# Performance work log

Hardware: AMD Instinct MI355X
Metric: run time of the kernel (lower is better)

## Reference

```python
import jax, jax.numpy as jnp
import numpy as np
import math

B, N, D_IN, D_OUT, H = 8, 1024, 512, 512, 8
DH = D_OUT // H  # 64
SCALE = math.sqrt(DH)

def setup_inputs() -> dict:
    key = jax.random.key(0)
    ks = jax.random.split(key, 10)
    s_in = 1.0 / math.sqrt(D_IN)
    s_out = 1.0 / math.sqrt(D_OUT)
    return {
        "x": jax.random.normal(ks[0], (B, N, D_IN), dtype=jnp.float32),
        "Wq": jax.random.uniform(ks[1], (D_IN, D_OUT), jnp.float32, -s_in, s_in),
        "bq": jnp.zeros((D_OUT,), jnp.float32),
        "Wk": jax.random.uniform(ks[2], (D_IN, D_OUT), jnp.float32, -s_in, s_in),
        "bk": jnp.zeros((D_OUT,), jnp.float32),
        "Wv": jax.random.uniform(ks[3], (D_IN, D_OUT), jnp.float32, -s_in, s_in),
        "bv": jnp.zeros((D_OUT,), jnp.float32),
        "Wo": jax.random.uniform(ks[4], (D_OUT, D_OUT), jnp.float32, -s_out, s_out),
        "bo": jnp.zeros((D_OUT,), jnp.float32),
        # external distance-based positional bias buffer (num_heads, N, N)
        "pos_bias": 0.01 * jax.random.normal(ks[5], (H, N, N), dtype=jnp.float32),
    }

def reference(x, Wq, bq, Wk, bk, Wv, bv, Wo, bo, pos_bias):
    Bx, Nx, _ = x.shape
    # QKV projections -> (B, H, N, DH)
    def split_heads(t):
        return t.reshape(Bx, Nx, H, DH).transpose(0, 2, 1, 3)
    q = split_heads(x @ Wq + bq)
    k = split_heads(x @ Wk + bk)
    v = split_heads(x @ Wv + bv)
    # scaled dot-product scores with additive positional bias
    scores = jnp.einsum('bhnd,bhmd->bhnm', q, k) / SCALE + pos_bias[None]
    attn = jax.nn.softmax(scores, axis=-1)  # dropout p=0 (eval)
    out = jnp.einsum('bhnm,bhmd->bhnd', attn, v)
    out = out.transpose(0, 2, 1, 3).reshape(Bx, Nx, D_OUT)  # concat heads
    return out @ Wo + bo
```

## Files before the change

### kernel.cpp

```cpp
#include <hip/hip_runtime.h>
#include <hip/hip_bf16.h>
#include <stdint.h>


typedef __attribute__((ext_vector_type(4))) float f32x4;
typedef __attribute__((ext_vector_type(8))) short s16x8;
typedef __attribute__((ext_vector_type(4))) unsigned short u16x4;
typedef __attribute__((ext_vector_type(8))) unsigned short u16x8;

union FragAB { s16x8 v; u16x4 h[2]; unsigned u[4]; };

#define LOG2E 1.44269504089f
#define QSCALE (0.125f * LOG2E)

__device__ __forceinline__ unsigned short f2b(float f) {
  unsigned u = __builtin_bit_cast(unsigned, f);
  u = (u + 0x7FFFu + ((u >> 16) & 1u)) >> 16;
  return (unsigned short)u;
}
__device__ __forceinline__ unsigned pack2(float lo, float hi) {
  return ((unsigned)f2b(hi) << 16) | (unsigned)f2b(lo);
}

__global__ __launch_bounds__(256) void prep_k(const float* __restrict__ x,
                                              unsigned short* __restrict__ xb,
                                              const float* __restrict__ W0,
                                              const float* __restrict__ W1,
                                              const float* __restrict__ W2,
                                              const float* __restrict__ W3,
                                              unsigned short* __restrict__ Wt) {
  __shared__ float ld[64][68];
  const int t = threadIdx.x;
  if (blockIdx.x < 4096) {
    int idx = blockIdx.x * 256 + t;
    f32x4 v = ((const f32x4*)x)[idx];
    u16x4 o;
#pragma unroll
    for (int j = 0; j < 4; j++) o[j] = f2b(v[j]);
    ((u16x4*)xb)[idx] = o;
    return;
  }
  const int bid2 = blockIdx.x - 4096;
  const int widx = bid2 >> 6;
  const int tile = bid2 & 63;
  const int trow = tile >> 3, tcol = tile & 7;
  const float* W = widx == 0 ? W0 : widx == 1 ? W1 : widx == 2 ? W2 : W3;
  const int r = t >> 2, cc = (t & 3) * 16;
  const float* src = W + (size_t)(trow * 64 + r) * 512 + tcol * 64 + cc;
#pragma unroll
  for (int u = 0; u < 4; u++)
    ((f32x4*)&ld[r][cc])[u] = ((const f32x4*)src)[u];
  __syncthreads();
  unsigned short* dst = Wt + ((size_t)widx << 18) + (size_t)(tcol * 64 + r) * 512 +
                        trow * 64 + cc;
#pragma unroll
  for (int u = 0; u < 4; u++) {
    u16x4 o;
#pragma unroll
    for (int e = 0; e < 4; e++) o[e] = f2b(ld[cc + u * 4 + e][r]);
    ((u16x4*)dst)[u] = o;
  }
}

__global__ __launch_bounds__(256, 2) void gemm_qkv_k(const unsigned short* __restrict__ A,
                                                     const unsigned short* __restrict__ Bt,
                                                     const float* __restrict__ bq,
                                                     const float* __restrict__ bk,
                                                     const float* __restrict__ bv,
                                                     unsigned short* __restrict__ outp) {
  __shared__ unsigned short At[2][128][36];
  __shared__ unsigned short Bts[2][128][36];
  const int tid = threadIdx.x;
  const int lane = tid & 63;
  const int w = tid >> 6;
  const int wm = w >> 1, wn = w & 1;
  const int g = lane >> 4, c = lane & 15;
  const int bn0 = (blockIdx.x % 12) * 128;
  const int bm0 = (blockIdx.x / 12) * 128;
  const int srow = tid >> 1;
  const int scol = (tid & 1) * 16;

  f32x4 acc[4][4];
#pragma unroll
  for (int i = 0; i < 4; i++)
#pragma unroll
    for (int j = 0; j < 4; j++) acc[i][j] = f32x4{0.f, 0.f, 0.f, 0.f};

  u16x4 ra[4], rb[4];
  auto ld = [&](int kt) {
    const u16x4* pa = (const u16x4*)(A + (size_t)(bm0 + srow) * 512 + kt * 32 + scol);
    const u16x4* pb = (const u16x4*)(Bt + (size_t)(bn0 + srow) * 512 + kt * 32 + scol);
#pragma unroll
    for (int j = 0; j < 4; j++) { ra[j] = pa[j]; rb[j] = pb[j]; }
  };
  auto st = [&](int b) {
    u16x4* da = (u16x4*)&At[b][srow][scol];
    u16x4* db = (u16x4*)&Bts[b][srow][scol];
#pragma unroll
    for (int j = 0; j < 4; j++) { da[j] = ra[j]; db[j] = rb[j]; }
  };

  ld(0); st(0);
  __syncthreads();

  for (int kt = 0; kt < 16; ++kt) {
    const int cb = kt & 1;
    if (kt < 15) ld(kt + 1);

    FragAB af[4], bf[4];
#pragma unroll
    for (int mi = 0; mi < 4; mi++) {
      const u16x4* p = (const u16x4*)&At[cb][wm * 64 + mi * 16 + c][g * 8];
      af[mi].h[0] = p[0]; af[mi].h[1] = p[1];
    }
#pragma unroll
    for (int ni = 0; ni < 4; ni++) {
      const u16x4* p = (const u16x4*)&Bts[cb][wn * 64 + ni * 16 + c][g * 8];
      bf[ni].h[0] = p[0]; bf[ni].h[1] = p[1];
    }
    __builtin_amdgcn_s_setprio(1);
#pragma unroll
    for (int mi = 0; mi < 4; mi++)
#pragma unroll
      for (int ni = 0; ni < 4; ni++)
        acc[mi][ni] = __builtin_amdgcn_mfma_f32_16x16x32_bf16(af[mi].v, bf[ni].v,
                                                              acc[mi][ni], 0, 0, 0);
    __builtin_amdgcn_s_setprio(0);

    if (kt < 15) {
      st(cb ^ 1);
      __syncthreads();
    }
  }

  const int qkv = (bn0 + wn * 64) >> 9;
  const float* bp = qkv == 0 ? bq : (qkv == 1 ? bk : bv);
  const float scale = qkv == 0 ? QSCALE : 1.0f;
#pragma unroll
  for (int mi = 0; mi < 4; mi++) {
#pragma unroll
    for (int ni = 0; ni < 4; ni++) {
      const int col = bn0 + wn * 64 + ni * 16 + c;
      const int c9 = col & 511;
      const float bvv = bp[c9];
#pragma unroll
      for (int m = 0; m < 4; m++) {
        const int row = bm0 + wm * 64 + mi * 16 + g * 4 + m;
        const float v = (acc[mi][ni][m] + bvv) * scale;
        const int b = row >> 10, n = row & 1023;
        const int hh = c9 >> 6, d = col & 63;
        outp[((size_t)qkv << 22) + ((size_t)((b << 3) + hh) << 16) +
             ((size_t)n << 6) + d] = f2b(v);
      }
    }
  }
}

__global__ __launch_bounds__(256, 2) void gemm_o_k(const unsigned short* __restrict__ A,
                                                   const unsigned short* __restrict__ Bt,
                                                   const float* __restrict__ bias,
                                                   float* __restrict__ outp) {
  __shared__ unsigned short At[2][128][36];
  __shared__ unsigned short Bts[2][128][36];
  const int tid = threadIdx.x;
  const int lane = tid & 63;
  const int w = tid >> 6;
  const int wm = w >> 1, wn = w & 1;
  const int g = lane >> 4, c = lane & 15;
  const int bn0 = (blockIdx.x & 3) * 128;
  const int bm0 = (blockIdx.x >> 2) * 128;
  const int srow = tid >> 1;
  const int scol = (tid & 1) * 16;

  f32x4 acc[4][4];
#pragma unroll
  for (int i = 0; i < 4; i++)
#pragma unroll
    for (int j = 0; j < 4; j++) acc[i][j] = f32x4{0.f, 0.f, 0.f, 0.f};

  u16x4 ra[4], rb[4];
  auto ld = [&](int kt) {
    const u16x4* pa = (const u16x4*)(A + (size_t)(bm0 + srow) * 512 + kt * 32 + scol);
    const u16x4* pb = (const u16x4*)(Bt + (size_t)(bn0 + srow) * 512 + kt * 32 + scol);
#pragma unroll
    for (int j = 0; j < 4; j++) { ra[j] = pa[j]; rb[j] = pb[j]; }
  };
  auto st = [&](int b) {
    u16x4* da = (u16x4*)&At[b][srow][scol];
    u16x4* db = (u16x4*)&Bts[b][srow][scol];
#pragma unroll
    for (int j = 0; j < 4; j++) { da[j] = ra[j]; db[j] = rb[j]; }
  };

  ld(0); st(0);
  __syncthreads();

  for (int kt = 0; kt < 16; ++kt) {
    const int cb = kt & 1;
    if (kt < 15) ld(kt + 1);

    FragAB af[4], bf[4];
#pragma unroll
    for (int mi = 0; mi < 4; mi++) {
      const u16x4* p = (const u16x4*)&At[cb][wm * 64 + mi * 16 + c][g * 8];
      af[mi].h[0] = p[0]; af[mi].h[1] = p[1];
    }
#pragma unroll
    for (int ni = 0; ni < 4; ni++) {
      const u16x4* p = (const u16x4*)&Bts[cb][wn * 64 + ni * 16 + c][g * 8];
      bf[ni].h[0] = p[0]; bf[ni].h[1] = p[1];
    }
    __builtin_amdgcn_s_setprio(1);
#pragma unroll
    for (int mi = 0; mi < 4; mi++)
#pragma unroll
      for (int ni = 0; ni < 4; ni++)
        acc[mi][ni] = __builtin_amdgcn_mfma_f32_16x16x32_bf16(af[mi].v, bf[ni].v,
                                                              acc[mi][ni], 0, 0, 0);
    __builtin_amdgcn_s_setprio(0);

    if (kt < 15) {
      st(cb ^ 1);
      __syncthreads();
    }
  }

#pragma unroll
  for (int mi = 0; mi < 4; mi++) {
#pragma unroll
    for (int ni = 0; ni < 4; ni++) {
      const int col = bn0 + wn * 64 + ni * 16 + c;
      const float bv = bias[col];
#pragma unroll
      for (int m = 0; m < 4; m++) {
        const int row = bm0 + wm * 64 + mi * 16 + g * 4 + m;
        outp[(size_t)row * 512 + col] = acc[mi][ni][m] + bv;
      }
    }
  }
}

__global__ __launch_bounds__(256, 2) void attn_k(const unsigned short* __restrict__ Qb,
                                                 const unsigned short* __restrict__ Kb,
                                                 const unsigned short* __restrict__ Vb,
                                                 const float* __restrict__ pos_bias,
                                                 unsigned short* __restrict__ ao) {
  __shared__ unsigned short Klds[2][64][68];
  __shared__ unsigned short Vtlds[2][64][68];
  __shared__ unsigned short Plds[4][32][68];

  const int tid = threadIdx.x;
  const int lane = tid & 63;
  const int w = tid >> 6;
  const int g = lane >> 4, c = lane & 15;
  const int L = blockIdx.x;
  const int qt = L >> 6;
  const int bh = (L & 7) + 8 * ((L >> 3) & 7);
  const int h = bh & 7;
  const size_t bhq = (size_t)bh << 16;
  const int q0 = qt * 128 + w * 32;

  FragAB aq[2][2];
#pragma unroll
  for (int mi = 0; mi < 2; mi++)
#pragma unroll
    for (int kk = 0; kk < 2; kk++) {
      const u16x4* p = (const u16x4*)(Qb + bhq + ((size_t)(q0 + mi * 16 + c) << 6) +
                                      kk * 32 + g * 8);
      aq[mi][kk].h[0] = p[0]; aq[mi][kk].h[1] = p[1];
    }

  f32x4 acco[2][4];
#pragma unroll
  for (int mi = 0; mi < 2; mi++)
#pragma unroll
    for (int nd = 0; nd < 4; nd++) acco[mi][nd] = f32x4{0.f, 0.f, 0.f, 0.f};
  float lsum[2] = {0.f, 0.f};

  const int krow = tid >> 3;
  const int kcol = (tid & 7) * 8;
  const int vd = tid & 63;
  const int vs = tid >> 6;

  u16x8 kr0, kr1;
  union { unsigned short s[16]; u16x8 v[2]; } vv;
  auto stageLoad = [&](int k0n) {
    kr0 = *(const u16x8*)(Kb + bhq + ((size_t)(k0n + krow) << 6) + kcol);
    kr1 = *(const u16x8*)(Kb + bhq + ((size_t)(k0n + krow + 32) << 6) + kcol);
    const unsigned short* pv = Vb + bhq + ((size_t)(k0n + vs * 16) << 6) + vd;
#pragma unroll
    for (int j = 0; j < 16; j++) vv.s[j] = pv[(size_t)j << 6];
  };
  auto stageWrite = [&](int b) {
    *(u16x8*)&Klds[b][krow][kcol] = kr0;
    *(u16x8*)&Klds[b][krow + 32][kcol] = kr1;
    *(u16x8*)&Vtlds[b][vd][vs * 16] = vv.v[0];
    *(u16x8*)&Vtlds[b][vd][vs * 16 + 8] = vv.v[1];
  };

  const float* pbB = pos_bias + ((size_t)h << 20) + ((size_t)(q0 + c) << 10) + 4 * g;

  stageLoad(0);
  stageWrite(0);
  __syncthreads();

  for (int kt = 0; kt < 16; ++kt) {
    const int buf = kt & 1;
    const int k0 = kt << 6;
    if (kt < 15) stageLoad(k0 + 64);

    f32x4 pb[2][4];
#pragma unroll
    for (int mi = 0; mi < 2; mi++)
#pragma unroll
      for (int ni = 0; ni < 4; ni++)
        pb[mi][ni] = *(const f32x4*)(pbB + (mi << 14) + k0 + 16 * ni);

    FragAB bk[4][2];
#pragma unroll
    for (int ni = 0; ni < 4; ni++)
#pragma unroll
      for (int kk = 0; kk < 2; kk++) {
        const u16x4* p = (const u16x4*)&Klds[buf][ni * 16 + c][kk * 32 + g * 8];
        bk[ni][kk].h[0] = p[0]; bk[ni][kk].h[1] = p[1];
      }
    f32x4 sT[2][4];
    __builtin_amdgcn_s_setprio(1);
#pragma unroll
    for (int mi = 0; mi < 2; mi++)
#pragma unroll
      for (int ni = 0; ni < 4; ni++) {
        f32x4 s = f32x4{0.f, 0.f, 0.f, 0.f};
        s = __builtin_amdgcn_mfma_f32_16x16x32_bf16(bk[ni][0].v, aq[mi][0].v, s, 0, 0, 0);
        s = __builtin_amdgcn_mfma_f32_16x16x32_bf16(bk[ni][1].v, aq[mi][1].v, s, 0, 0, 0);
        sT[mi][ni] = s;
      }
    __builtin_amdgcn_s_setprio(0);

#pragma unroll
    for (int mi = 0; mi < 2; mi++)
#pragma unroll
      for (int ni = 0; ni < 4; ni++) {
        const float p0 = __builtin_amdgcn_exp2f(fmaf(pb[mi][ni][0], LOG2E, sT[mi][ni][0]));
        const float p1 = __builtin_amdgcn_exp2f(fmaf(pb[mi][ni][1], LOG2E, sT[mi][ni][1]));
        const float p2 = __builtin_amdgcn_exp2f(fmaf(pb[mi][ni][2], LOG2E, sT[mi][ni][2]));
        const float p3 = __builtin_amdgcn_exp2f(fmaf(pb[mi][ni][3], LOG2E, sT[mi][ni][3]));
        lsum[mi] += (p0 + p1) + (p2 + p3);
        uint2 two;
        two.x = pack2(p0, p1);
        two.y = pack2(p2, p3);
        *(uint2*)&Plds[w][mi * 16 + c][16 * ni + 4 * g] = two;
      }

    asm volatile("s_waitcnt lgkmcnt(0)" ::: "memory");

    FragAB paf[2][2], vb2[4][2];
#pragma unroll
    for (int mi = 0; mi < 2; mi++)
#pragma unroll
      for (int kc = 0; kc < 2; kc++) {
        const u16x4* p = (const u16x4*)&Plds[w][mi * 16 + c][kc * 32 + g * 8];
        paf[mi][kc].h[0] = p[0]; paf[mi][kc].h[1] = p[1];
      }
#pragma unroll
    for (int nd = 0; nd < 4; nd++)
#pragma unroll
      for (int kc = 0; kc < 2; kc++) {
        const u16x4* p = (const u16x4*)&Vtlds[buf][nd * 16 + c][kc * 32 + g * 8];
        vb2[nd][kc].h[0] = p[0]; vb2[nd][kc].h[1] = p[1];
      }
    __builtin_amdgcn_s_setprio(1);
#pragma unroll
    for (int mi = 0; mi < 2; mi++)
#pragma unroll
      for (int nd = 0; nd < 4; nd++) {
        acco[mi][nd] = __builtin_amdgcn_mfma_f32_16x16x32_bf16(paf[mi][0].v, vb2[nd][0].v,
                                                               acco[mi][nd], 0, 0, 0);
        acco[mi][nd] = __builtin_amdgcn_mfma_f32_16x16x32_bf16(paf[mi][1].v, vb2[nd][1].v,
                                                               acco[mi][nd], 0, 0, 0);
      }
    __builtin_amdgcn_s_setprio(0);

    if (kt < 15) {
      stageWrite(buf ^ 1);
      __syncthreads();
    }
  }

  const int b = bh >> 3;
#pragma unroll
  for (int mi = 0; mi < 2; mi++) {
    float l = lsum[mi];
    l += __shfl_xor(l, 16);
    l += __shfl_xor(l, 32);
    const float inv_c = 1.f / l;
#pragma unroll
    for (int m = 0; m < 4; m++) {
      const float invm = __shfl(inv_c, g * 4 + m);
      const int n = q0 + mi * 16 + g * 4 + m;
#pragma unroll
      for (int nd = 0; nd < 4; nd++) {
        ao[((size_t)(b * 1024 + n) << 9) + h * 64 + nd * 16 + c] =
            f2b(acco[mi][nd][m] * invm);
      }
    }
  }
}

extern "C" void kernel_launch(void* const* d_in, const int* in_sizes, int n_in,
                              void* d_out, int out_size, void* d_ws, size_t ws_size,
                              hipStream_t stream) {
  (void)in_sizes; (void)n_in; (void)out_size; (void)ws_size;
  const float* x  = (const float*)d_in[0];
  const float* Wq = (const float*)d_in[1];
  const float* bq = (const float*)d_in[2];
  const float* Wk = (const float*)d_in[3];
  const float* bk = (const float*)d_in[4];
  const float* Wv = (const float*)d_in[5];
  const float* bv = (const float*)d_in[6];
  const float* Wo = (const float*)d_in[7];
  const float* bo = (const float*)d_in[8];
  const float* pbias = (const float*)d_in[9];

  char* p = (char*)d_ws;
  unsigned short* xb  = (unsigned short*)p; p += (size_t)8192 * 512 * 2;
  unsigned short* WT  = (unsigned short*)p; p += (size_t)4 * 512 * 512 * 2;
  unsigned short* Qb  = (unsigned short*)p; p += (size_t)3 * 64 * 1024 * 64 * 2;
  unsigned short* AO  = (unsigned short*)p;

  unsigned short* WoT = WT + (size_t)3 * 512 * 512;
  unsigned short* Kb  = Qb + (size_t)64 * 1024 * 64;
  unsigned short* Vb  = Kb + (size_t)64 * 1024 * 64;

  prep_k<<<4352, 256, 0, stream>>>(x, xb, Wq, Wk, Wv, Wo, WT);
  gemm_qkv_k<<<768, 256, 0, stream>>>(xb, WT, bq, bk, bv, Qb);
  attn_k<<<512, 256, 0, stream>>>(Qb, Kb, Vb, pbias, AO);
  gemm_o_k<<<256, 256, 0, stream>>>(AO, WoT, bo, (float*)d_out);
}
```

Baseline: 88.09 us.

## Write V transposed from QKV GEMM and widen output GEMM to 512 threads

The QKV projection epilogue now stores V in a [bh][d][n] layout, so the attention kernel can stage V^T into LDS with contiguous 16-byte loads instead of 16 strided scalar loads per thread. The output GEMM is launched with 512 threads per block, each wave covering 32 rows, and uses single 16-byte vector loads for staging. The P-to-bf16 packing switches to the library conversion intrinsic. The transposed V store from the GEMM epilogue is scattered, which may add write cost there.

```diff
diff --git a/kernel.cpp b/kernel.cpp
--- a/kernel.cpp
+++ b/kernel.cpp
@@ -18,8 +18,10 @@
   u = (u + 0x7FFFu + ((u >> 16) & 1u)) >> 16;
   return (unsigned short)u;
 }
-__device__ __forceinline__ unsigned pack2(float lo, float hi) {
-  return ((unsigned)f2b(hi) << 16) | (unsigned)f2b(lo);
+__device__ __forceinline__ unsigned pack2f(float lo, float hi) {
+  const unsigned short a = __builtin_bit_cast(unsigned short, __float2bfloat16(lo));
+  const unsigned short b = __builtin_bit_cast(unsigned short, __float2bfloat16(hi));
+  return ((unsigned)b << 16) | (unsigned)a;
 }
 
 __global__ __launch_bounds__(256) void prep_k(const float* __restrict__ x,
@@ -149,14 +151,19 @@
         const float v = (acc[mi][ni][m] + bvv) * scale;
         const int b = row >> 10, n = row & 1023;
         const int hh = c9 >> 6, d = col & 63;
-        outp[((size_t)qkv << 22) + ((size_t)((b << 3) + hh) << 16) +
-             ((size_t)n << 6) + d] = f2b(v);
-      }
-    }
-  }
-}
-
-__global__ __launch_bounds__(256, 2) void gemm_o_k(const unsigned short* __restrict__ A,
+        if (qkv == 2) {
+          outp[((size_t)2 << 22) + ((size_t)((b << 3) + hh) << 16) +
+               ((size_t)d << 10) + n] = f2b(v);
+        } else {
+          outp[((size_t)qkv << 22) + ((size_t)((b << 3) + hh) << 16) +
+               ((size_t)n << 6) + d] = f2b(v);
+        }
+      }
+    }
+  }
+}
+
+__global__ __launch_bounds__(512, 2) void gemm_o_k(const unsigned short* __restrict__ A,
                                                    const unsigned short* __restrict__ Bt,
                                                    const float* __restrict__ bias,
                                                    float* __restrict__ outp) {
@@ -169,27 +176,23 @@
   const int g = lane >> 4, c = lane & 15;
   const int bn0 = (blockIdx.x & 3) * 128;
   const int bm0 = (blockIdx.x >> 2) * 128;
-  const int srow = tid >> 1;
-  const int scol = (tid & 1) * 16;
-
-  f32x4 acc[4][4];
-#pragma unroll
-  for (int i = 0; i < 4; i++)
+  const int srow = tid >> 2;
+  const int scol = (tid & 3) * 8;
+
+  f32x4 acc[2][4];
+#pragma unroll
+  for (int i = 0; i < 2; i++)
 #pragma unroll
     for (int j = 0; j < 4; j++) acc[i][j] = f32x4{0.f, 0.f, 0.f, 0.f};
 
-  u16x4 ra[4], rb[4];
+  u16x8 ra, rb;
   auto ld = [&](int kt) {
-    const u16x4* pa = (const u16x4*)(A + (size_t)(bm0 + srow) * 512 + kt * 32 + scol);
-    const u16x4* pb = (const u16x4*)(Bt + (size_t)(bn0 + srow) * 512 + kt * 32 + scol);
-#pragma unroll
-    for (int j = 0; j < 4; j++) { ra[j] = pa[j]; rb[j] = pb[j]; }
+    ra = *(const u16x8*)(A + (size_t)(bm0 + srow) * 512 + kt * 32 + scol);
+    rb = *(const u16x8*)(Bt + (size_t)(bn0 + srow) * 512 + kt * 32 + scol);
   };
   auto st = [&](int b) {
-    u16x4* da = (u16x4*)&At[b][srow][scol];
-    u16x4* db = (u16x4*)&Bts[b][srow][scol];
-#pragma unroll
-    for (int j = 0; j < 4; j++) { da[j] = ra[j]; db[j] = rb[j]; }
+    *(u16x8*)&At[b][srow][scol] = ra;
+    *(u16x8*)&Bts[b][srow][scol] = rb;
   };
 
   ld(0); st(0);
@@ -199,10 +202,10 @@
     const int cb = kt & 1;
     if (kt < 15) ld(kt + 1);
 
-    FragAB af[4], bf[4];
-#pragma unroll
-    for (int mi = 0; mi < 4; mi++) {
-      const u16x4* p = (const u16x4*)&At[cb][wm * 64 + mi * 16 + c][g * 8];
+    FragAB af[2], bf[4];
+#pragma unroll
+    for (int mi = 0; mi < 2; mi++) {
+      const u16x4* p = (const u16x4*)&At[cb][wm * 32 + mi * 16 + c][g * 8];
       af[mi].h[0] = p[0]; af[mi].h[1] = p[1];
     }
 #pragma unroll
@@ -212,7 +215,7 @@
     }
     __builtin_amdgcn_s_setprio(1);
 #pragma unroll
-    for (int mi = 0; mi < 4; mi++)
+    for (int mi = 0; mi < 2; mi++)
 #pragma unroll
       for (int ni = 0; ni < 4; ni++)
         acc[mi][ni] = __builtin_amdgcn_mfma_f32_16x16x32_bf16(af[mi].v, bf[ni].v,
@@ -226,14 +229,14 @@
   }
 
 #pragma unroll
-  for (int mi = 0; mi < 4; mi++) {
+  for (int mi = 0; mi < 2; mi++) {
 #pragma unroll
     for (int ni = 0; ni < 4; ni++) {
       const int col = bn0 + wn * 64 + ni * 16 + c;
       const float bv = bias[col];
 #pragma unroll
       for (int m = 0; m < 4; m++) {
-        const int row = bm0 + wm * 64 + mi * 16 + g * 4 + m;
+        const int row = bm0 + wm * 32 + mi * 16 + g * 4 + m;
         outp[(size_t)row * 512 + col] = acc[mi][ni][m] + bv;
       }
     }
@@ -242,7 +245,7 @@
 
 __global__ __launch_bounds__(256, 2) void attn_k(const unsigned short* __restrict__ Qb,
                                                  const unsigned short* __restrict__ Kb,
-                                                 const unsigned short* __restrict__ Vb,
+                                                 const unsigned short* __restrict__ Vt,
                                                  const float* __restrict__ pos_bias,
                                                  unsigned short* __restrict__ ao) {
   __shared__ unsigned short Klds[2][64][68];
@@ -277,25 +280,23 @@
     for (int nd = 0; nd < 4; nd++) acco[mi][nd] = f32x4{0.f, 0.f, 0.f, 0.f};
   float lsum[2] = {0.f, 0.f};
 
-  const int krow = tid >> 3;
-  const int kcol = (tid & 7) * 8;
-  const int vd = tid & 63;
-  const int vs = tid >> 6;
-
-  u16x8 kr0, kr1;
-  union { unsigned short s[16]; u16x8 v[2]; } vv;
+  const int srow = tid >> 2;
+  const int scol = (tid & 3) * 16;
+  const unsigned short* pK = Kb + bhq + ((size_t)srow << 6) + scol;
+  const unsigned short* pV = Vt + bhq + ((size_t)srow << 10) + scol;
+
+  u16x8 kr0, kr1, vr0, vr1;
   auto stageLoad = [&](int k0n) {
-    kr0 = *(const u16x8*)(Kb + bhq + ((size_t)(k0n + krow) << 6) + kcol);
-    kr1 = *(const u16x8*)(Kb + bhq + ((size_t)(k0n + krow + 32) << 6) + kcol);
-    const unsigned short* pv = Vb + bhq + ((size_t)(k0n + vs * 16) << 6) + vd;
-#pragma unroll
-    for (int j = 0; j < 16; j++) vv.s[j] = pv[(size_t)j << 6];
+    const u16x8* a = (const u16x8*)(pK + ((size_t)k0n << 6));
+    kr0 = a[0]; kr1 = a[1];
+    const u16x8* b = (const u16x8*)(pV + k0n);
+    vr0 = b[0]; vr1 = b[1];
   };
   auto stageWrite = [&](int b) {
-    *(u16x8*)&Klds[b][krow][kcol] = kr0;
-    *(u16x8*)&Klds[b][krow + 32][kcol] = kr1;
-    *(u16x8*)&Vtlds[b][vd][vs * 16] = vv.v[0];
-    *(u16x8*)&Vtlds[b][vd][vs * 16 + 8] = vv.v[1];
+    *(u16x8*)&Klds[b][srow][scol] = kr0;
+    *(u16x8*)&Klds[b][srow][scol + 8] = kr1;
+    *(u16x8*)&Vtlds[b][srow][scol] = vr0;
+    *(u16x8*)&Vtlds[b][srow][scol + 8] = vr1;
   };
 
   const float* pbB = pos_bias + ((size_t)h << 20) + ((size_t)(q0 + c) << 10) + 4 * g;
@@ -347,8 +348,8 @@
         const float p3 = __builtin_amdgcn_exp2f(fmaf(pb[mi][ni][3], LOG2E, sT[mi][ni][3]));
         lsum[mi] += (p0 + p1) + (p2 + p3);
         uint2 two;
-        two.x = pack2(p0, p1);
-        two.y = pack2(p2, p3);
+        two.x = pack2f(p0, p1);
+        two.y = pack2f(p2, p3);
         *(uint2*)&Plds[w][mi * 16 + c][16 * ni + 4 * g] = two;
       }
 
@@ -435,5 +436,5 @@
   prep_k<<<4352, 256, 0, stream>>>(x, xb, Wq, Wk, Wv, Wo, WT);
   gemm_qkv_k<<<768, 256, 0, stream>>>(xb, WT, bq, bk, bv, Qb);
   attn_k<<<512, 256, 0, stream>>>(Qb, Kb, Vb, pbias, AO);
-  gemm_o_k<<<256, 256, 0, stream>>>(AO, WoT, bo, (float*)d_out);
-}
+  gemm_o_k<<<256, 512, 0, stream>>>(AO, WoT, bo, (float*)d_out);
+}
```

Result: no change. 88.84 us (+0.8%).
